# Kernel optimization log

Measured on AMD Instinct MI355X. Metric: run time of the kernel, lower is better.

The kernel has to match this reference:

```python
import jax, jax.numpy as jnp
import numpy as np

FRAME_LENGTH = 64   # hop size (init default)
GAIN = 0.01         # attenuate_gain


def setup_inputs() -> dict:
    key = jax.random.key(0)
    k1, k2 = jax.random.split(key)
    B, F, L = 32, 4000, 65
    noise_filter = jax.random.uniform(k1, (B, F, L), dtype=jnp.float32)
    noise = jax.random.uniform(k2, (B, F, FRAME_LENGTH), dtype=jnp.float32)
    return {"noise_filter": noise_filter, "noise": noise}


def reference(noise_filter, noise):
    B, F, L = noise_filter.shape
    hop = FRAME_LENGTH
    N = 2 * L - 1                       # odd-length zero-phase IR
    K = hop + 2 * L - 2                 # FFT-conv output length per frame
    # periodic Hann window (torch.hann_window default)
    win = 0.5 * (1.0 - jnp.cos(2.0 * jnp.pi * jnp.arange(N, dtype=jnp.float32) / N))
    # zero-phase IR from real (zero-imag) frequency response, then make linear phase
    ir = jnp.fft.irfft(noise_filter, n=N, axis=-1)          # [B,F,N]
    ir = jnp.roll(ir, L - 1, axis=-1) * win                 # windowed linear-phase IR
    H = jnp.fft.rfft(jnp.pad(ir, ((0, 0), (0, 0), (0, hop - 1))), axis=-1)   # [B,F,K//2+1]
    n = noise * 2.0 - 1.0                                   # uniform [-1,1)
    Nspec = jnp.fft.rfft(jnp.pad(n, ((0, 0), (0, 0), (0, 2 * L - 2))), axis=-1)
    frames = jnp.fft.irfft(Nspec * H, n=K, axis=-1) * GAIN  # [B,F,K]
    # overlap-add with stride = hop
    out_len = (F - 1) * hop + K
    idx = (jnp.arange(F)[:, None] * hop + jnp.arange(K)[None, :]).reshape(-1)
    out = jnp.zeros((B, out_len), frames.dtype).at[:, idx].add(frames.reshape(B, -1))
    return out
```

## Files before the change

kernel.cpp:

```cpp
#include <hip/hip_runtime.h>
#include <math.h>

typedef float v2f __attribute__((ext_vector_type(2)));

#define B_    32
#define F_    4000
#define L_    65
#define N_    129
#define HOP_  64
#define K_    192
#define GF_   8
#define WAVES_ 4
#define OUTLEN_ ((F_-1)*HOP_ + K_)
#define GAIN_ 0.01f
#define BLKS_PER_B_ (F_/(GF_*WAVES_))


__global__ __launch_bounds__(256, 2) void filtered_noise_kernel(
    const float* __restrict__ nfilt,
    const float* __restrict__ noise,
    float* __restrict__ out)
{
    __shared__ float costab[N_];
    __shared__ float irp[WAVES_][260];

    const int tid  = threadIdx.x;
    const int lane = tid & 63;
    const int wid  = __builtin_amdgcn_readfirstlane(tid >> 6);

    for (int i = tid; i < N_; i += 256)
        costab[i] = (float)cos((double)i * (2.0 * M_PI / 129.0));

    float* ir = irp[wid];
    for (int i = lane; i < 260; i += 64) ir[i] = 0.0f;

    __syncthreads();

    const int b  = blockIdx.x / BLKS_PER_B_;
    const int g  = (blockIdx.x % BLKS_PER_B_) * WAVES_ + wid;
    const int f0 = g * GF_;

    const int   t     = lane + 1;
    const float scale = 2.0f / 129.0f;
    const float cA = 0.5f * (1.0f - costab[64 - t]) * scale;
    const float cB = 0.5f * (1.0f - costab[64 + t]) * scale;
    const float c0 = 0.5f * (1.0f - costab[64]) * scale;

    const float c1 = costab[t];
    const float tc = 2.0f * c1;
    float sdA[4], sdB[4];
    sdA[0] = 1.0f;                 sdB[0] = c1;
    sdA[1] = costab[(16*t) % N_];  sdB[1] = costab[(17*t) % N_];
    sdA[2] = costab[(32*t) % N_];  sdB[2] = costab[(33*t) % N_];
    sdA[3] = costab[(48*t) % N_];  sdB[3] = costab[(49*t) % N_];

    const float* Xf = nfilt + (size_t)(b * F_ + f0) * L_;
    const float* Zf = noise + (size_t)(b * F_ + f0) * HOP_ + lane;
    float*       op = out + (size_t)b * OUTLEN_ + (size_t)f0 * HOP_ + lane;

    const float* pb = ir + lane;

    v2f wab = {0.0f, 0.0f};
    float wc = 0.0f;

    #pragma unroll 1
    for (int i = 0; i < GF_; ++i) {
        float zc = Zf[0];
        zc = fmaf(2.0f, zc, -1.0f);

        float x0 = Xf[0];
        float a = 0.5f * x0;
        float s = 0.5f * x0;
        #pragma unroll
        for (int c = 0; c < 4; ++c) {
            float ckm1 = sdA[c], ck = sdB[c];
            float aa = 0.0f, ss = 0.0f;
            #pragma unroll
            for (int q = 0; q < 16; ++q) {
                float x = Xf[c * 16 + q + 1];
                aa = fmaf(x, ck, aa);
                ss += x;
                float cn = fmaf(tc, ck, -ckm1);
                ckm1 = ck; ck = cn;
            }
            a += aa; s += ss;
        }

        __builtin_amdgcn_sched_barrier(0);
        ir[128 - t] = cA * a;
        ir[128 + t] = cB * a;
        if (lane == 0) ir[128] = c0 * s;
        __builtin_amdgcn_sched_barrier(0);

        #pragma unroll
        for (int j = 0; j < HOP_; ++j) {
            float njs = __uint_as_float(
                __builtin_amdgcn_readlane(__float_as_uint(zc), j));
            v2f njv = {njs, njs};
            v2f pv  = {pb[64 - j], pb[128 - j]};
            wab = njv * pv + wab;
            wc  = fmaf(njs, pb[192 - j], wc);
        }
        __builtin_amdgcn_sched_barrier(0);

        float v = wab.x * GAIN_;
        if (i < 2) atomicAdd(op, v); else *op = v;
        op += HOP_;
        wab.x = wab.y; wab.y = wc; wc = 0.0f;
        Xf += L_; Zf += HOP_;
    }
    atomicAdd(op, wab.x * GAIN_);
    atomicAdd(op + HOP_, wab.y * GAIN_);
}

extern "C" void kernel_launch(void* const* d_in, const int* in_sizes, int n_in,
                              void* d_out, int out_size, void* d_ws, size_t ws_size,
                              hipStream_t stream) {
    const float* nfilt = (const float*)d_in[0];
    const float* noise = (const float*)d_in[1];
    float* out = (float*)d_out;

    hipMemsetAsync(d_out, 0, (size_t)out_size * sizeof(float), stream);

    dim3 grid(B_ * BLKS_PER_B_);
    dim3 block(256);
    filtered_noise_kernel<<<grid, block, 0, stream>>>(nfilt, noise, out);
}
```

Measured before the change: 232.6 us.

## Halve frames per wave and split convolution accumulators into four chains

Frames per wave drop from 8 to 4, which doubles the grid so more waves can run and hide latency. The price is more atomic adds at group boundaries and recomputing the cosine table in more blocks. The inner convolution loop no longer uses packed v2f FMAs. It now processes two taps per step with scalar FMAs spread over four independent accumulator chains to shorten dependency latency. This uses more registers, gives up the packed-math throughput, and changes the floating-point summation order.

After: 258.0 us. 1.11x slower.

```diff
diff --git a/kernel.cpp b/kernel.cpp
--- a/kernel.cpp
+++ b/kernel.cpp
@@ -1,7 +1,5 @@
 #include <hip/hip_runtime.h>
 #include <math.h>
-
-typedef float v2f __attribute__((ext_vector_type(2)));
 
 #define B_    32
 #define F_    4000
@@ -9,7 +7,7 @@
 #define N_    129
 #define HOP_  64
 #define K_    192
-#define GF_   8
+#define GF_   4
 #define WAVES_ 4
 #define OUTLEN_ ((F_-1)*HOP_ + K_)
 #define GAIN_ 0.01f
@@ -60,8 +58,7 @@
 
     const float* pb = ir + lane;
 
-    v2f wab = {0.0f, 0.0f};
-    float wc = 0.0f;
+    float wa[4] = {0,0,0,0}, wb[4] = {0,0,0,0}, wc[4] = {0,0,0,0};
 
     #pragma unroll 1
     for (int i = 0; i < GF_; ++i) {
@@ -93,24 +90,32 @@
         __builtin_amdgcn_sched_barrier(0);
 
         #pragma unroll
-        for (int j = 0; j < HOP_; ++j) {
-            float njs = __uint_as_float(
+        for (int p = 0; p < 32; ++p) {
+            const int j = 2 * p;
+            const int c = p & 3;
+            float nj0 = __uint_as_float(
                 __builtin_amdgcn_readlane(__float_as_uint(zc), j));
-            v2f njv = {njs, njs};
-            v2f pv  = {pb[64 - j], pb[128 - j]};
-            wab = njv * pv + wab;
-            wc  = fmaf(njs, pb[192 - j], wc);
+            float nj1 = __uint_as_float(
+                __builtin_amdgcn_readlane(__float_as_uint(zc), j + 1));
+            float a1 = pb[63 - j],  a0 = pb[64 - j];
+            float b1 = pb[127 - j], b0 = pb[128 - j];
+            float d1 = pb[191 - j], d0 = pb[192 - j];
+            wa[c] = fmaf(nj0, a0, wa[c]);  wa[c] = fmaf(nj1, a1, wa[c]);
+            wb[c] = fmaf(nj0, b0, wb[c]);  wb[c] = fmaf(nj1, b1, wb[c]);
+            wc[c] = fmaf(nj0, d0, wc[c]);  wc[c] = fmaf(nj1, d1, wc[c]);
         }
         __builtin_amdgcn_sched_barrier(0);
 
-        float v = wab.x * GAIN_;
-        if (i < 2) atomicAdd(op, v); else *op = v;
+        float va = ((wa[0] + wa[1]) + (wa[2] + wa[3])) * GAIN_;
+        if (i < 2) atomicAdd(op, va); else *op = va;
         op += HOP_;
-        wab.x = wab.y; wab.y = wc; wc = 0.0f;
+        #pragma unroll
+        for (int c = 0; c < 4; ++c) { wa[c] = wb[c]; wb[c] = wc[c]; wc[c] = 0.0f; }
         Xf += L_; Zf += HOP_;
     }
-    atomicAdd(op, wab.x * GAIN_);
-    atomicAdd(op + HOP_, wab.y * GAIN_);
+    atomicAdd(op,        ((wa[0] + wa[1]) + (wa[2] + wa[3])) * GAIN_);
+    atomicAdd(op + HOP_, ((wb[0] + wb[1]) + (wb[2] + wb[3])) * GAIN_);
+
 }
 
 extern "C" void kernel_launch(void* const* d_in, const int* in_sizes, int n_in,
```
